# Optimization experiments

Hardware: AMD Instinct MI355X
Metric: run time of the kernel (lower is better)

Reference implementation:

```python
import jax, jax.numpy as jnp
import numpy as np
import math

N = 512            # batch
D = 512            # in_features (embedding dim)
C = 50000          # out_features (num classes)
S = 30.0           # scale
M = 0.5            # margin
COS_M = math.cos(M)
SIN_M = math.sin(M)
TH = math.cos(math.pi - M)
MM = math.sin(math.pi - M) * M


def _l2norm(x, eps=1e-12):
    # torch F.normalize: x / max(||x||_2, eps) along dim=1
    n = jnp.sqrt(jnp.sum(x * x, axis=1, keepdims=True))
    return x / jnp.maximum(n, eps)


def setup_inputs() -> dict:
    key = jax.random.key(0)
    k1, k2, k3 = jax.random.split(key, 3)
    logits = jax.random.normal(k1, (N, D), dtype=jnp.float32)
    labels = jax.random.randint(k2, (N,), 0, C, dtype=jnp.int64)
    # xavier_uniform over (C, D): bound = sqrt(6/(C+D))
    bound = math.sqrt(6.0 / (C + D))
    weight = jax.random.uniform(k3, (C, D), dtype=jnp.float32, minval=-bound, maxval=bound)
    return {"logits": logits, "labels": labels, "weight": weight}


def reference(logits, labels, weight):
    x = _l2norm(logits)                      # [N, D]
    w = _l2norm(weight)                      # [C, D]
    cosine = jnp.einsum('nd,cd->nc', x, w)   # [N, C]
    sine = jnp.sqrt(jnp.clip(1.0 + 1e-7 - cosine * cosine, 0.0, 1.0))
    phi = cosine * COS_M - sine * SIN_M
    # easy_margin=False branch
    phi = jnp.where(cosine > TH, phi, cosine - MM)
    onehot = jax.nn.one_hot(labels, C, dtype=cosine.dtype)  # [N, C]
    output = (onehot * phi + (1.0 - onehot) * cosine) * S
    # CrossEntropyLoss(reduction='none') then .mean()
    logp = jax.nn.log_softmax(output, axis=1)
    loss_per = -jnp.take_along_axis(logp, labels[:, None], axis=1)[:, 0]
    loss = jnp.mean(loss_per)
    return output, loss
```

## Files before the change

### kernel.cpp

```cpp
#include <hip/hip_runtime.h>
#include <stdint.h>

#define N_B   512
#define D_K   512
#define C_N   50000
#define C_PAD 50048
#define BM    128
#define BN    128
#define BK    32
#define NCB   391
#define NWG   (NCB * 4)

#define S_SCALE 30.0f
#define COS_Mc  0.87758256189037276f
#define SIN_Mc  0.47942553860420301f
#define TH_Cc  (-0.87758256189037276f)
#define MM_Cc   0.23971276930210156f
#define NEG_BIG (-3.0e38f)

typedef __attribute__((ext_vector_type(8))) __bf16 bf16x8;
typedef __attribute__((ext_vector_type(4))) float  f32x4;

__device__ __forceinline__ unsigned short f2bf(float f) {
    union { float f; unsigned u; } v; v.f = f;
    unsigned r = v.u + 0x7FFFu + ((v.u >> 16) & 1u);
    return (unsigned short)(r >> 16);
}

__device__ __forceinline__ void gl2lds16(const void* g, void* l) {
    __builtin_amdgcn_global_load_lds(
        (__attribute__((address_space(1))) unsigned int*)(g),
        (__attribute__((address_space(3))) unsigned int*)(l),
        16, 0, 0);
}

__global__ __launch_bounds__(256) void prep_kernel(
        const float* __restrict__ src, unsigned short* __restrict__ dstb,
        float* __restrict__ inv, int nvalid, int ntotal)
{
    int wave = threadIdx.x >> 6, lane = threadIdx.x & 63;
    int row = blockIdx.x * 4 + wave;
    if (row >= ntotal) return;
    unsigned short* dst = dstb + (size_t)row * D_K + lane * 8;
    if (row < nvalid) {
        const float4* s4 = (const float4*)(src + (size_t)row * D_K) + lane * 2;
        float4 a = s4[0], b = s4[1];
        float ss = a.x*a.x + a.y*a.y + a.z*a.z + a.w*a.w
                 + b.x*b.x + b.y*b.y + b.z*b.z + b.w*b.w;
        #pragma unroll
        for (int off = 32; off >= 1; off >>= 1) ss += __shfl_xor(ss, off, 64);
        if (lane == 0) inv[row] = 1.0f / fmaxf(sqrtf(ss), 1e-12f);
        uint4 o;
        o.x = (unsigned)f2bf(a.x) | ((unsigned)f2bf(a.y) << 16);
        o.y = (unsigned)f2bf(a.z) | ((unsigned)f2bf(a.w) << 16);
        o.z = (unsigned)f2bf(b.x) | ((unsigned)f2bf(b.y) << 16);
        o.w = (unsigned)f2bf(b.z) | ((unsigned)f2bf(b.w) << 16);
        *(uint4*)dst = o;
    } else {
        *(uint4*)dst = make_uint4(0u, 0u, 0u, 0u);
        if (lane == 0) inv[row] = 0.0f;
    }
}

__global__ __launch_bounds__(256) void gemm_margin_kernel(
        const unsigned short* __restrict__ xb, const unsigned short* __restrict__ wb,
        const float* __restrict__ invx, const float* __restrict__ invw,
        const int* __restrict__ labels, float* __restrict__ out,
        float* __restrict__ m_part, float* __restrict__ s_part)
{
    const int orig = blockIdx.x;
    const int qch = NWG >> 3, rch = NWG & 7;
    const int xcd = orig & 7, idx = orig >> 3;
    const int wg = (xcd < rch ? xcd * (qch + 1)
                              : rch * (qch + 1) + (xcd - rch) * qch) + idx;
    const int cb = wg >> 2, rb = wg & 3;
    const int m0 = rb * BM, c0 = cb * BN;
    const int tid = threadIdx.x;
    const int lane = tid & 63, wave = tid >> 6;
    const int wm = wave >> 1, wn = wave & 1;
    const int l15 = lane & 15, q = lane >> 4;

    __shared__ __align__(16) unsigned short As[2][BM * BK];
    __shared__ __align__(16) unsigned short Bs[2][BN * BK];
    __shared__ float s_invx[BM];
    __shared__ float s_invw[BN];
    __shared__ int   s_lab[BM];
    __shared__ float sm[2][BM];
    __shared__ float ssm[2][BM];

    f32x4 zero4 = {0.f, 0.f, 0.f, 0.f};
    f32x4 acc[4][4];
    #pragma unroll
    for (int i = 0; i < 4; i++)
        #pragma unroll
        for (int j = 0; j < 4; j++) acc[i][j] = zero4;

    const int srow   = tid >> 2;
    const int pchunk = tid & 3;
    const int lch0 = pchunk ^ ((srow >> 1) & 3);
    const int lch1 = pchunk ^ (((srow + 64) >> 1) & 3);

    const unsigned short* gA0 = xb + (size_t)(m0 + srow)      * D_K + lch0 * 8;
    const unsigned short* gA1 = xb + (size_t)(m0 + srow + 64) * D_K + lch1 * 8;
    const unsigned short* gB0 = wb + (size_t)(c0 + srow)      * D_K + lch0 * 8;
    const unsigned short* gB1 = wb + (size_t)(c0 + srow + 64) * D_K + lch1 * 8;

    const int off0 = srow * BK + pchunk * 8;
    const int off1 = (srow + 64) * BK + pchunk * 8;

    int aoff[4], boff[4];
    #pragma unroll
    for (int i = 0; i < 4; i++) {
        int Ra = wm * 64 + i * 16 + l15;
        aoff[i] = Ra * BK + (q ^ ((Ra >> 1) & 3)) * 8;
        int Rb = wn * 64 + i * 16 + l15;
        boff[i] = Rb * BK + (q ^ ((Rb >> 1) & 3)) * 8;
    }

#define STAGE(b, k0) do {                       \
        gl2lds16(gA0 + (k0), &As[b][off0]);     \
        gl2lds16(gA1 + (k0), &As[b][off1]);     \
        gl2lds16(gB0 + (k0), &Bs[b][off0]);     \
        gl2lds16(gB1 + (k0), &Bs[b][off1]);     \
    } while (0)

#define COMPUTE(b) do {                                                       \
        bf16x8 af_[4], bf_[4];                                                \
        _Pragma("unroll")                                                     \
        for (int i = 0; i < 4; i++) af_[i] = *(const bf16x8*)(&As[b][aoff[i]]); \
        _Pragma("unroll")                                                     \
        for (int i = 0; i < 4; i++) bf_[i] = *(const bf16x8*)(&Bs[b][boff[i]]); \
        _Pragma("unroll")                                                     \
        for (int mi = 0; mi < 4; mi++)                                        \
            _Pragma("unroll")                                                 \
            for (int ni = 0; ni < 4; ni++)                                    \
                acc[mi][ni] = __builtin_amdgcn_mfma_f32_16x16x32_bf16(        \
                                  af_[mi], bf_[ni], acc[mi][ni], 0, 0, 0);    \
    } while (0)

    STAGE(0, 0);
    if (tid < BM) {
        s_invx[tid] = invx[m0 + tid];
        s_lab[tid]  = labels[m0 + tid];
        s_invw[tid] = invw[c0 + tid];
    }
    __syncthreads();

    #pragma unroll
    for (int t = 0; t < 16; ++t) {
        const int cur = t & 1;
        if (t < 15) STAGE(cur ^ 1, (t + 1) * BK);
        COMPUTE(cur);
        __syncthreads();
    }
#undef STAGE
#undef COMPUTE

    #pragma unroll
    for (int mi = 0; mi < 4; mi++) {
        #pragma unroll
        for (int r = 0; r < 4; r++) {
            int lrow = wm * 64 + mi * 16 + q * 4 + r;
            int grow = m0 + lrow;
            float ivx = s_invx[lrow];
            int lab = s_lab[lrow];
            float tv[4]; bool ok[4];
            float vmax = NEG_BIG;
            #pragma unroll
            for (int ni = 0; ni < 4; ni++) {
                int lcol = wn * 64 + ni * 16 + l15;
                int gcol = c0 + lcol;
                float cosv = acc[mi][ni][r] * ivx * s_invw[lcol];
                float o;
                if (gcol == lab) {
                    float s2 = 1.0f + 1e-7f - cosv * cosv;
                    s2 = fminf(fmaxf(s2, 0.0f), 1.0f);
                    float phi = cosv * COS_Mc - sqrtf(s2) * SIN_Mc;
                    if (!(cosv > TH_Cc)) phi = cosv - MM_Cc;
                    o = S_SCALE * phi;
                } else {
                    o = S_SCALE * cosv;
                }
                ok[ni] = (gcol < C_N);
                tv[ni] = o;
                if (ok[ni]) {
                    __builtin_nontemporal_store(o, &out[(size_t)grow * C_N + gcol]);
                    vmax = fmaxf(vmax, o);
                }
            }
            #pragma unroll
            for (int off = 1; off < 16; off <<= 1)
                vmax = fmaxf(vmax, __shfl_xor(vmax, off, 64));
            float vs = 0.f;
            #pragma unroll
            for (int ni = 0; ni < 4; ni++)
                if (ok[ni]) vs += __expf(tv[ni] - vmax);
            #pragma unroll
            for (int off = 1; off < 16; off <<= 1)
                vs += __shfl_xor(vs, off, 64);
            if (l15 == 0) { sm[wn][lrow] = vmax; ssm[wn][lrow] = vs; }
        }
    }
    __syncthreads();
    if (tid < BM) {
        float m1 = sm[0][tid], s1 = ssm[0][tid];
        float m2 = sm[1][tid], s2 = ssm[1][tid];
        float M = fmaxf(m1, m2);
        float S = s1 * __expf(m1 - M) + s2 * __expf(m2 - M);
        m_part[(size_t)(m0 + tid) * NCB + cb] = M;
        s_part[(size_t)(m0 + tid) * NCB + cb] = S;
    }
}

__global__ void rowreduce_kernel(
        const float* __restrict__ m_part, const float* __restrict__ s_part,
        const float* __restrict__ out, const int* __restrict__ labels,
        float* __restrict__ lossp)
{
    int row = blockIdx.x;
    int lane = threadIdx.x;
    float m = NEG_BIG, s = 0.f;
    for (int j = lane; j < NCB; j += 64) {
        float m2 = m_part[(size_t)row * NCB + j];
        float s2 = s_part[(size_t)row * NCB + j];
        float M = fmaxf(m, m2);
        s = s * __expf(m - M) + s2 * __expf(m2 - M);
        m = M;
    }
    #pragma unroll
    for (int off = 1; off < 64; off <<= 1) {
        float om = __shfl_xor(m, off, 64);
        float os = __shfl_xor(s, off, 64);
        float M = fmaxf(m, om);
        s = s * __expf(m - M) + os * __expf(om - M);
        m = M;
    }
    if (lane == 0) {
        float logZ = m + logf(s);
        int lab = labels[row];
        lossp[row] = logZ - out[(size_t)row * C_N + lab];
    }
}

__global__ void loss_kernel(const float* __restrict__ lossp, float* __restrict__ loss_out) {
    int t = threadIdx.x;
    float v = lossp[t] + lossp[t + 256];
    #pragma unroll
    for (int off = 32; off >= 1; off >>= 1) v += __shfl_xor(v, off, 64);
    __shared__ float part[4];
    if ((t & 63) == 0) part[t >> 6] = v;
    __syncthreads();
    if (t == 0) loss_out[0] = (part[0] + part[1] + part[2] + part[3]) * (1.0f / 512.0f);
}

extern "C" void kernel_launch(void* const* d_in, const int* in_sizes, int n_in,
                              void* d_out, int out_size, void* d_ws, size_t ws_size,
                              hipStream_t stream)
{
    const float* x      = (const float*)d_in[0];
    const int*   labels = (const int*)d_in[1];
    const float* w      = (const float*)d_in[2];
    float* out = (float*)d_out;
    float* loss_out = out + (size_t)N_B * C_N;

    char* ws = (char*)d_ws;
    size_t off = 0;
    unsigned short* xb = (unsigned short*)(ws + off); off += (size_t)N_B * D_K * 2;
    unsigned short* wb = (unsigned short*)(ws + off); off += (size_t)C_PAD * D_K * 2;
    float* invx   = (float*)(ws + off); off += (size_t)N_B * 4;
    float* invw   = (float*)(ws + off); off += (size_t)C_PAD * 4;
    float* m_part = (float*)(ws + off); off += (size_t)N_B * NCB * 4;
    float* s_part = (float*)(ws + off); off += (size_t)N_B * NCB * 4;
    float* lossp  = (float*)(ws + off); off += (size_t)N_B * 4;

    prep_kernel<<<N_B / 4, 256, 0, stream>>>(x, xb, invx, N_B, N_B);
    prep_kernel<<<C_PAD / 4, 256, 0, stream>>>(w, wb, invw, C_N, C_PAD);
    gemm_margin_kernel<<<dim3(NWG), 256, 0, stream>>>(xb, wb, invx, invw, labels,
                                                      out, m_part, s_part);
    rowreduce_kernel<<<N_B, 64, 0, stream>>>(m_part, s_part, out, labels, lossp);
    loss_kernel<<<1, 256, 0, stream>>>(lossp, loss_out);
}
```

Baseline: 254.1 us.

## Load GEMM operands directly from global, merge prep kernels, atomic loss accumulation

New measurement: 312.7 us. 1.23x slower.

```diff
diff --git a/kernel.cpp b/kernel.cpp
--- a/kernel.cpp
+++ b/kernel.cpp
@@ -27,20 +27,22 @@
     return (unsigned short)(r >> 16);
 }
 
-__device__ __forceinline__ void gl2lds16(const void* g, void* l) {
-    __builtin_amdgcn_global_load_lds(
-        (__attribute__((address_space(1))) unsigned int*)(g),
-        (__attribute__((address_space(3))) unsigned int*)(l),
-        16, 0, 0);
-}
-
-__global__ __launch_bounds__(256) void prep_kernel(
-        const float* __restrict__ src, unsigned short* __restrict__ dstb,
-        float* __restrict__ inv, int nvalid, int ntotal)
-{
+__global__ __launch_bounds__(256) void prep_all_kernel(
+        const float* __restrict__ x, unsigned short* __restrict__ xb,
+        float* __restrict__ invx,
+        const float* __restrict__ w, unsigned short* __restrict__ wb,
+        float* __restrict__ invw, float* __restrict__ loss_out)
+{
+    if (blockIdx.x == 0 && threadIdx.x == 0) *loss_out = 0.f;
     int wave = threadIdx.x >> 6, lane = threadIdx.x & 63;
-    int row = blockIdx.x * 4 + wave;
-    if (row >= ntotal) return;
+    const float* src; unsigned short* dstb; float* inv; int row, nvalid;
+    if (blockIdx.x < 128) {
+        src = x; dstb = xb; inv = invx; nvalid = N_B;
+        row = blockIdx.x * 4 + wave;
+    } else {
+        src = w; dstb = wb; inv = invw; nvalid = C_N;
+        row = (blockIdx.x - 128) * 4 + wave;
+    }
     unsigned short* dst = dstb + (size_t)row * D_K + lane * 8;
     if (row < nvalid) {
         const float4* s4 = (const float4*)(src + (size_t)row * D_K) + lane * 2;
@@ -62,7 +64,7 @@
     }
 }
 
-__global__ __launch_bounds__(256) void gemm_margin_kernel(
+__global__ __launch_bounds__(256, 3) void gemm_margin_kernel(
         const unsigned short* __restrict__ xb, const unsigned short* __restrict__ wb,
         const float* __restrict__ invx, const float* __restrict__ invw,
         const int* __restrict__ labels, float* __restrict__ out,
@@ -80,14 +82,18 @@
     const int wm = wave >> 1, wn = wave & 1;
     const int l15 = lane & 15, q = lane >> 4;
 
-    __shared__ __align__(16) unsigned short As[2][BM * BK];
-    __shared__ __align__(16) unsigned short Bs[2][BN * BK];
     __shared__ float s_invx[BM];
     __shared__ float s_invw[BN];
     __shared__ int   s_lab[BM];
     __shared__ float sm[2][BM];
     __shared__ float ssm[2][BM];
 
+    if (tid < BM) {
+        s_invx[tid] = invx[m0 + tid];
+        s_lab[tid]  = labels[m0 + tid];
+        s_invw[tid] = invw[c0 + tid];
+    }
+
     f32x4 zero4 = {0.f, 0.f, 0.f, 0.f};
     f32x4 acc[4][4];
     #pragma unroll
@@ -95,66 +101,27 @@
         #pragma unroll
         for (int j = 0; j < 4; j++) acc[i][j] = zero4;
 
-    const int srow   = tid >> 2;
-    const int pchunk = tid & 3;
-    const int lch0 = pchunk ^ ((srow >> 1) & 3);
-    const int lch1 = pchunk ^ (((srow + 64) >> 1) & 3);
-
-    const unsigned short* gA0 = xb + (size_t)(m0 + srow)      * D_K + lch0 * 8;
-    const unsigned short* gA1 = xb + (size_t)(m0 + srow + 64) * D_K + lch1 * 8;
-    const unsigned short* gB0 = wb + (size_t)(c0 + srow)      * D_K + lch0 * 8;
-    const unsigned short* gB1 = wb + (size_t)(c0 + srow + 64) * D_K + lch1 * 8;
-
-    const int off0 = srow * BK + pchunk * 8;
-    const int off1 = (srow + 64) * BK + pchunk * 8;
-
-    int aoff[4], boff[4];
-    #pragma unroll
-    for (int i = 0; i < 4; i++) {
-        int Ra = wm * 64 + i * 16 + l15;
-        aoff[i] = Ra * BK + (q ^ ((Ra >> 1) & 3)) * 8;
-        int Rb = wn * 64 + i * 16 + l15;
-        boff[i] = Rb * BK + (q ^ ((Rb >> 1) & 3)) * 8;
-    }
-
-#define STAGE(b, k0) do {                       \
-        gl2lds16(gA0 + (k0), &As[b][off0]);     \
-        gl2lds16(gA1 + (k0), &As[b][off1]);     \
-        gl2lds16(gB0 + (k0), &Bs[b][off0]);     \
-        gl2lds16(gB1 + (k0), &Bs[b][off1]);     \
-    } while (0)
-
-#define COMPUTE(b) do {                                                       \
-        bf16x8 af_[4], bf_[4];                                                \
-        _Pragma("unroll")                                                     \
-        for (int i = 0; i < 4; i++) af_[i] = *(const bf16x8*)(&As[b][aoff[i]]); \
-        _Pragma("unroll")                                                     \
-        for (int i = 0; i < 4; i++) bf_[i] = *(const bf16x8*)(&Bs[b][boff[i]]); \
-        _Pragma("unroll")                                                     \
-        for (int mi = 0; mi < 4; mi++)                                        \
-            _Pragma("unroll")                                                 \
-            for (int ni = 0; ni < 4; ni++)                                    \
-                acc[mi][ni] = __builtin_amdgcn_mfma_f32_16x16x32_bf16(        \
-                                  af_[mi], bf_[ni], acc[mi][ni], 0, 0, 0);    \
-    } while (0)
-
-    STAGE(0, 0);
-    if (tid < BM) {
-        s_invx[tid] = invx[m0 + tid];
-        s_lab[tid]  = labels[m0 + tid];
-        s_invw[tid] = invw[c0 + tid];
-    }
+    const unsigned short* a_base = xb + (size_t)(m0 + wm * 64 + l15) * D_K + q * 8;
+    const unsigned short* b_base = wb + (size_t)(c0 + wn * 64 + l15) * D_K + q * 8;
+
+    #pragma unroll 2
+    for (int k0 = 0; k0 < D_K; k0 += BK) {
+        bf16x8 a[4], b[4];
+        #pragma unroll
+        for (int i = 0; i < 4; i++)
+            a[i] = *(const bf16x8*)(a_base + (size_t)i * 16 * D_K + k0);
+        #pragma unroll
+        for (int i = 0; i < 4; i++)
+            b[i] = *(const bf16x8*)(b_base + (size_t)i * 16 * D_K + k0);
+        #pragma unroll
+        for (int mi = 0; mi < 4; mi++)
+            #pragma unroll
+            for (int ni = 0; ni < 4; ni++)
+                acc[mi][ni] = __builtin_amdgcn_mfma_f32_16x16x32_bf16(
+                                  a[mi], b[ni], acc[mi][ni], 0, 0, 0);
+    }
+
     __syncthreads();
-
-    #pragma unroll
-    for (int t = 0; t < 16; ++t) {
-        const int cur = t & 1;
-        if (t < 15) STAGE(cur ^ 1, (t + 1) * BK);
-        COMPUTE(cur);
-        __syncthreads();
-    }
-#undef STAGE
-#undef COMPUTE
 
     #pragma unroll
     for (int mi = 0; mi < 4; mi++) {
@@ -184,7 +151,7 @@
                 ok[ni] = (gcol < C_N);
                 tv[ni] = o;
                 if (ok[ni]) {
-                    __builtin_nontemporal_store(o, &out[(size_t)grow * C_N + gcol]);
+                    out[(size_t)grow * C_N + gcol] = o;
                     vmax = fmaxf(vmax, o);
                 }
             }
@@ -215,7 +182,7 @@
 __global__ void rowreduce_kernel(
         const float* __restrict__ m_part, const float* __restrict__ s_part,
         const float* __restrict__ out, const int* __restrict__ labels,
-        float* __restrict__ lossp)
+        float* __restrict__ loss_out)
 {
     int row = blockIdx.x;
     int lane = threadIdx.x;
@@ -238,19 +205,8 @@
     if (lane == 0) {
         float logZ = m + logf(s);
         int lab = labels[row];
-        lossp[row] = logZ - out[(size_t)row * C_N + lab];
-    }
-}
-
-__global__ void loss_kernel(const float* __restrict__ lossp, float* __restrict__ loss_out) {
-    int t = threadIdx.x;
-    float v = lossp[t] + lossp[t + 256];
-    #pragma unroll
-    for (int off = 32; off >= 1; off >>= 1) v += __shfl_xor(v, off, 64);
-    __shared__ float part[4];
-    if ((t & 63) == 0) part[t >> 6] = v;
-    __syncthreads();
-    if (t == 0) loss_out[0] = (part[0] + part[1] + part[2] + part[3]) * (1.0f / 512.0f);
+        atomicAdd(loss_out, (logZ - out[(size_t)row * C_N + lab]) * (1.0f / 512.0f));
+    }
 }
 
 extern "C" void kernel_launch(void* const* d_in, const int* in_sizes, int n_in,
@@ -271,12 +227,10 @@
     float* invw   = (float*)(ws + off); off += (size_t)C_PAD * 4;
     float* m_part = (float*)(ws + off); off += (size_t)N_B * NCB * 4;
     float* s_part = (float*)(ws + off); off += (size_t)N_B * NCB * 4;
-    float* lossp  = (float*)(ws + off); off += (size_t)N_B * 4;
-
-    prep_kernel<<<N_B / 4, 256, 0, stream>>>(x, xb, invx, N_B, N_B);
-    prep_kernel<<<C_PAD / 4, 256, 0, stream>>>(w, wb, invw, C_N, C_PAD);
+
+    prep_all_kernel<<<128 + C_PAD / 4, 256, 0, stream>>>(x, xb, invx, w, wb, invw,
+                                                         loss_out);
     gemm_margin_kernel<<<dim3(NWG), 256, 0, stream>>>(xb, wb, invx, invw, labels,
                                                       out, m_part, s_part);
-    rowreduce_kernel<<<N_B, 64, 0, stream>>>(m_part, s_part, out, labels, lossp);
-    loss_kernel<<<1, 256, 0, stream>>>(lossp, loss_out);
-}
+    rowreduce_kernel<<<N_B, 64, 0, stream>>>(m_part, s_part, out, labels, loss_out);
+}
```
